# Kernel optimization log

Measured on AMD Instinct MI355X. Metric: run time of the kernel, lower is better.

## Reference

```python
import jax, jax.numpy as jnp
import numpy as np

TEMPERATURE = 0.1
B, T, D = 8, 1024, 1024
NEG_INF = -1e30

def setup_inputs() -> dict:
    key = jax.random.key(0)
    k1, k2, k3 = jax.random.split(key, 3)
    features = jax.random.normal(k1, (B, T, D), dtype=jnp.float32)
    masks = jax.random.bernoulli(k2, 0.05, (B, 1, T, T)).astype(jnp.float32)
    input_coords_length = jax.random.randint(k3, (B,), T // 2, T - 1)  # int32
    return {"features": features, "masks": masks, "input_coords_length": input_coords_length}


def _sup_con_loss(feat, mask, L):
    # feat: [T, D], mask: [T, T] float, L: scalar int valid length (slice [:L, :L])
    Tn = feat.shape[0]
    dt = feat.dtype
    vr = jnp.arange(Tn) < L                              # valid rows/cols [T]
    valid2d = (vr[:, None] & vr[None, :]).astype(dt)     # [T, T]
    dot = jnp.matmul(feat, feat.T) / TEMPERATURE         # [T, T]
    dot = jnp.where(vr[None, :], dot, NEG_INF)           # exclude padded cols from max
    logits = dot - jax.lax.stop_gradient(jnp.max(dot, axis=-1, keepdims=True))
    logits_mask = (1.0 - jnp.eye(Tn, dtype=dt)) * valid2d  # off-diagonal, in-slice
    exp_logits = jnp.exp(logits) * logits_mask
    m = mask * valid2d
    # negative_mask = 1-mask; entries < 1 zeroed (binary mask -> indicator of mask==0)
    neg = 1.0 - m
    neg = jnp.where(neg < 1.0, 0.0, neg) * valid2d
    # positive_mask = mask with entries > 0 set to 1
    pos = jnp.where(m > 0, 1.0, m)
    neg_denom = jnp.sum(exp_logits * neg, axis=-1, keepdims=True)
    pos_denom = jax.lax.stop_gradient(jnp.sum(exp_logits * pos, axis=-1, keepdims=True))
    log_prob = logits - jnp.log(neg_denom + pos_denom + 1e-6)
    m2 = m * logits_mask
    mean_log_prob_pos = (m2 * log_prob).sum(-1) / (m2.sum(-1) + 1e-6)  # [T]
    # mean over the L valid rows only (matches .mean() on the sliced tensor)
    return -jnp.sum(jnp.where(vr, mean_log_prob_pos, 0.0)) / L.astype(dt)


def _is_valid(mask, L):
    # valid sample iff sliced mask differs from eye(L) with [0,0]=0
    Tn = mask.shape[0]
    vr = jnp.arange(Tn) < L
    valid2d = (vr[:, None] & vr[None, :]).astype(mask.dtype)
    sanity = jnp.eye(Tn, dtype=mask.dtype).at[0, 0].set(0.0) * valid2d
    return jnp.any((mask * valid2d) != sanity)


def reference(features, masks, input_coords_length):
    L = input_coords_length + 1                      # [B]
    mask0 = masks[:, 0]                              # [B, T, T] (num_layers asserted == 1)
    losses = jax.vmap(_sup_con_loss)(features, mask0, L)   # [B]
    valid = jax.vmap(_is_valid)(mask0, L)                  # [B] bool
    vbs = jnp.maximum(jnp.sum(valid.astype(features.dtype)), 1.0)
    return jnp.sum(losses) / vbs
```

## Files before the change

### kernel.cpp

```cpp
#include <hip/hip_runtime.h>
#include <hip/hip_bf16.h>
#include <stdint.h>

#define T_DIM 1024
#define B_DIM 8

typedef __attribute__((ext_vector_type(8))) short short8;
typedef __attribute__((ext_vector_type(4))) float f32x4;

__device__ inline void gll16(const void* g, void* l) {
  __builtin_amdgcn_global_load_lds((__attribute__((address_space(1))) void*)g,
                                   (__attribute__((address_space(3))) void*)l,
                                   16, 0, 0);
}

__global__ __launch_bounds__(256) void convert_kernel(const float* __restrict__ F,
                                                      __hip_bfloat16* __restrict__ Fb) {
  const int t = blockIdx.x * 256 + threadIdx.x;
  const float4 v = ((const float4*)F)[t];
  union { __hip_bfloat16 h[4]; uint64_t u; } p;
  p.h[0] = __float2bfloat16(v.x);
  p.h[1] = __float2bfloat16(v.y);
  p.h[2] = __float2bfloat16(v.z);
  p.h[3] = __float2bfloat16(v.w);
  ((uint64_t*)Fb)[t] = p.u;
}

__global__ __launch_bounds__(512, 4) void fused_kernel(const __hip_bfloat16* __restrict__ Fb,
                                                       const float* __restrict__ M,
                                                       const int* __restrict__ icl,
                                                       float* __restrict__ part) {
  const int id = blockIdx.x;
  const int b  = id & 7;
  const int rt = (id >> 3) & 7;
  const int ct = id >> 6;
  const int L  = icl[b] + 1;
  if (rt * 128 >= L || ct * 128 >= L) return;

  __shared__ char smem[65536];
  __hip_bfloat16* As = (__hip_bfloat16*)smem;
  __hip_bfloat16* Bs = (__hip_bfloat16*)(smem + 32768);
  float* rp = (float*)smem;
  float* rp_m = rp;
  float* rp_d = rp + 512;
  float* rp_s = rp + 1024;
  float* rp_c = rp + 1536;
  float* rp_b = rp + 2048;

  const __hip_bfloat16* F = Fb + ((size_t)b << 20);
  const int tid  = threadIdx.x;
  const int lane = tid & 63;
  const int wave = tid >> 6;
  const int wrow = (wave >> 2) * 64;
  const int wcol = (wave & 3) * 32;
  const int row0 = rt * 128;
  const int col0 = ct * 128;

  const int fr = lane & 15;
  const int q  = lane >> 4;
  const int sl8 = (q ^ ((fr >> 1) & 3)) * 8;

  const int srow = tid >> 2;
  const int sgk  = (((tid & 3) ^ ((tid >> 3) & 3)) * 8);

  const size_t arow = (size_t)(row0 + srow) * T_DIM + sgk;
  const size_t brow = (size_t)(col0 + srow) * T_DIM + sgk;

  auto stage = [&](int buf, int step) {
    const int kb = step << 6;
#pragma unroll
    for (int p = 0; p < 2; p++)
      gll16(F + arow + kb + p * 32, As + buf * 8192 + p * 4096 + tid * 8);
#pragma unroll
    for (int p = 0; p < 2; p++)
      gll16(F + brow + kb + p * 32, Bs + buf * 8192 + p * 4096 + tid * 8);
  };

  stage(0, 0);
  stage(1, 1);

  f32x4 acc[4][2];
#pragma unroll
  for (int i = 0; i < 4; i++)
#pragma unroll
    for (int j = 0; j < 2; j++) acc[i][j] = (f32x4){0.f, 0.f, 0.f, 0.f};

#pragma unroll
  for (int t = 0; t < 16; ++t) {
    const int cur = t & 1;
    if (t < 15) { asm volatile("s_waitcnt vmcnt(4)" ::: "memory"); }
    else        { asm volatile("s_waitcnt vmcnt(0)" ::: "memory"); }
    __builtin_amdgcn_s_barrier();
    __builtin_amdgcn_sched_barrier(0);

    short8 af[2][4], bfr[2][2];
    const __hip_bfloat16* Ab = As + cur * 8192;
    const __hip_bfloat16* Bb = Bs + cur * 8192;
#pragma unroll
    for (int kk = 0; kk < 2; kk++) {
#pragma unroll
      for (int tt = 0; tt < 4; tt++)
        af[kk][tt] = *(const short8*)(Ab + kk * 4096 + (wrow + tt * 16 + fr) * 32 + sl8);
#pragma unroll
      for (int j = 0; j < 2; j++)
        bfr[kk][j] = *(const short8*)(Bb + kk * 4096 + (wcol + j * 16 + fr) * 32 + sl8);
    }
    asm volatile("s_waitcnt lgkmcnt(0)" ::: "memory");
    __builtin_amdgcn_sched_barrier(0);
    __builtin_amdgcn_s_barrier();
    __builtin_amdgcn_sched_barrier(0);

    if (t < 14) stage(cur, t + 2);

    __builtin_amdgcn_s_setprio(1);
#pragma unroll
    for (int kk = 0; kk < 2; kk++)
#pragma unroll
      for (int ti = 0; ti < 4; ti++)
#pragma unroll
        for (int tj = 0; tj < 2; tj++)
          acc[ti][tj] = __builtin_amdgcn_mfma_f32_16x16x32_bf16(bfr[kk][tj], af[kk][ti], acc[ti][tj], 0, 0, 0);
    __builtin_amdgcn_s_setprio(0);
  }
  __syncthreads();

  uint32_t mbits = 0;
  {
    const float* Mb = M + ((size_t)b << 20);
    union { float4 v; float f[4]; } mv[4][2];
#pragma unroll
    for (int ti = 0; ti < 4; ti++) {
      const int grow = row0 + wrow + ti * 16 + fr;
#pragma unroll
      for (int tj = 0; tj < 2; tj++)
        mv[ti][tj].v = *(const float4*)(Mb + ((size_t)grow << 10) + col0 + wcol + tj * 16 + q * 4);
    }
#pragma unroll
    for (int ti = 0; ti < 4; ti++)
#pragma unroll
      for (int tj = 0; tj < 2; tj++)
#pragma unroll
        for (int r = 0; r < 4; r++)
          mbits |= ((mv[ti][tj].f[r] != 0.f) ? 1u : 0u) << (ti * 8 + tj * 4 + r);
  }

#pragma unroll
  for (int ti = 0; ti < 4; ti++) {
    const int lrow = wrow + ti * 16 + fr;
    const int grow = row0 + lrow;
    float s[2][4];
#pragma unroll
    for (int tj = 0; tj < 2; tj++)
#pragma unroll
      for (int r = 0; r < 4; r++) {
        const int gcol = col0 + wcol + tj * 16 + q * 4 + r;
        s[tj][r] = (gcol < L) ? acc[ti][tj][r] * 10.0f : -1e30f;
      }
    float m = s[0][0];
#pragma unroll
    for (int tj = 0; tj < 2; tj++)
#pragma unroll
      for (int r = 0; r < 4; r++) m = fmaxf(m, s[tj][r]);
    m = fmaxf(m, __shfl_xor(m, 16, 64));
    m = fmaxf(m, __shfl_xor(m, 32, 64));

    float den = 0.f, msum = 0.f, cnt = 0.f, badf = 0.f;
#pragma unroll
    for (int tj = 0; tj < 2; tj++)
#pragma unroll
      for (int r = 0; r < 4; r++) {
        const int gcol = col0 + wcol + tj * 16 + q * 4 + r;
        if (gcol < L) {
          const float mk = (float)((mbits >> (ti * 8 + tj * 4 + r)) & 1u);
          if (gcol != grow) {
            den  += __expf(s[tj][r] - m);
            msum += mk * s[tj][r];
            cnt  += mk;
          }
          const float sane = (gcol == grow && grow != 0) ? 1.f : 0.f;
          badf = fmaxf(badf, (mk != sane) ? 1.f : 0.f);
        }
      }
    den  += __shfl_xor(den, 16, 64);  den  += __shfl_xor(den, 32, 64);
    msum += __shfl_xor(msum, 16, 64); msum += __shfl_xor(msum, 32, 64);
    cnt  += __shfl_xor(cnt, 16, 64);  cnt  += __shfl_xor(cnt, 32, 64);
    badf = fmaxf(badf, __shfl_xor(badf, 16, 64));
    badf = fmaxf(badf, __shfl_xor(badf, 32, 64));

    if (q == 0) {
      const int slot = wave & 3;
      rp_m[lrow * 4 + slot] = m;    rp_d[lrow * 4 + slot] = den;
      rp_s[lrow * 4 + slot] = msum; rp_c[lrow * 4 + slot] = cnt;
      rp_b[lrow * 4 + slot] = badf;
    }
  }
  __syncthreads();

  if (tid < 128) {
    float m = -1e30f;
#pragma unroll
    for (int s = 0; s < 4; s++) m = fmaxf(m, rp_m[tid * 4 + s]);
    float den = 0.f, msum = 0.f, cnt = 0.f, badf = 0.f;
#pragma unroll
    for (int s = 0; s < 4; s++) {
      den  += rp_d[tid * 4 + s] * __expf(rp_m[tid * 4 + s] - m);
      msum += rp_s[tid * 4 + s];
      cnt  += rp_c[tid * 4 + s];
      badf  = fmaxf(badf, rp_b[tid * 4 + s]);
    }
    float* p = part + ((((size_t)b * 1024 + row0 + tid) * 8) + ct) * 5;
    p[0] = m; p[1] = den; p[2] = msum; p[3] = cnt; p[4] = badf;
  }
}

__global__ __launch_bounds__(256) void reduce_kernel(const float* __restrict__ part,
                                                     const int* __restrict__ icl,
                                                     float* __restrict__ blk_sum,
                                                     int* __restrict__ blk_bad) {
  const int blk = blockIdx.x;
  const int row = blk * 256 + threadIdx.x;
  const int b = row >> 10;
  const int i = row & 1023;
  const int L = icl[b] + 1;
  float rv = 0.f;
  int bad = 0;
  if (i < L) {
    const float* p = part + (size_t)row * 40;
    const int ns = (L + 127) >> 7;
    float m = -1e30f;
    for (int s = 0; s < ns; s++) m = fmaxf(m, p[s * 5 + 0]);
    float den = 0.f, msum = 0.f, cnt = 0.f, badf = 0.f;
    for (int s = 0; s < ns; s++) {
      den  += p[s * 5 + 1] * __expf(p[s * 5 + 0] - m);
      msum += p[s * 5 + 2];
      cnt  += p[s * 5 + 3];
      badf  = fmaxf(badf, p[s * 5 + 4]);
    }
    const float A = msum - cnt * m;
    const float mlpp = (A - cnt * __logf(den + 1e-6f)) / (cnt + 1e-6f);
    rv = -mlpp / (float)L;
    bad = badf > 0.f ? 1 : 0;
  }
  const int tid  = threadIdx.x;
  const int lane = tid & 63;
  const int wave = tid >> 6;
  for (int o = 32; o > 0; o >>= 1) rv += __shfl_down(rv, o, 64);
  const int wbad = (__ballot(bad) != 0ull) ? 1 : 0;
  __shared__ float sred[4];
  __shared__ int bred[4];
  if (lane == 0) { sred[wave] = rv; bred[wave] = wbad; }
  __syncthreads();
  if (tid == 0) {
    blk_sum[blk] = sred[0] + sred[1] + sred[2] + sred[3];
    blk_bad[blk] = bred[0] | bred[1] | bred[2] | bred[3];
  }
}

__global__ __launch_bounds__(64) void final_kernel(const float* __restrict__ blk_sum,
                                                   const int* __restrict__ blk_bad,
                                                   float* __restrict__ out) {
  const int tid = threadIdx.x;
  float v = (tid < 32) ? blk_sum[tid] : 0.f;
  for (int o = 32; o > 0; o >>= 1) v += __shfl_down(v, o, 64);
  if (tid == 0) {
    int vcount = 0;
    for (int bb = 0; bb < B_DIM; bb++) {
      const int any = blk_bad[bb * 4] | blk_bad[bb * 4 + 1] |
                      blk_bad[bb * 4 + 2] | blk_bad[bb * 4 + 3];
      vcount += any ? 1 : 0;
    }
    out[0] = v / fmaxf((float)vcount, 1.0f);
  }
}

extern "C" void kernel_launch(void* const* d_in, const int* in_sizes, int n_in,
                              void* d_out, int out_size, void* d_ws, size_t ws_size,
                              hipStream_t stream) {
  const float* feat = (const float*)d_in[0];
  const float* mask = (const float*)d_in[1];
  const int*   icl  = (const int*)d_in[2];
  float* out = (float*)d_out;

  char* ws = (char*)d_ws;
  __hip_bfloat16* Fb = (__hip_bfloat16*)ws;
  float* part    = (float*)(ws + (16u << 20));
  float* blk_sum = (float*)(ws + (18u << 20));
  int*   blk_bad = (int*)(ws + (18u << 20) + 512);

  convert_kernel<<<dim3(8192), dim3(256), 0, stream>>>(feat, Fb);
  fused_kernel<<<dim3(512), dim3(512), 0, stream>>>(Fb, mask, icl, part);
  reduce_kernel<<<dim3(32), dim3(256), 0, stream>>>(part, icl, blk_sum, blk_bad);
  final_kernel<<<dim3(1), dim3(64), 0, stream>>>(blk_sum, blk_bad, out);
}
```

Measured before the change: 120.4 us.

## Fuse fp32-to-bf16 conversion into GEMM tile loads and share tile on diagonal blocks

Removes the separate convert kernel and its bf16 workspace. The fused kernel now loads fp32 features into registers, converts them to bf16 and writes them to LDS, using a register-staged double buffer in place of direct global-to-LDS loads. Diagonal tiles (row tile equals column tile) load and write only the A tile and reuse it as B. This saves a kernel launch and a full write and re-read of the bf16 copy. In exchange, each block reads twice the bytes in fp32, the conversion is redone by every block that uses a tile, and more registers are live, which may hurt occupancy or latency hiding.

```diff
diff --git a/kernel.cpp b/kernel.cpp
--- a/kernel.cpp
+++ b/kernel.cpp
@@ -8,25 +8,16 @@
 typedef __attribute__((ext_vector_type(8))) short short8;
 typedef __attribute__((ext_vector_type(4))) float f32x4;
 
-__device__ inline void gll16(const void* g, void* l) {
-  __builtin_amdgcn_global_load_lds((__attribute__((address_space(1))) void*)g,
-                                   (__attribute__((address_space(3))) void*)l,
-                                   16, 0, 0);
-}
-
-__global__ __launch_bounds__(256) void convert_kernel(const float* __restrict__ F,
-                                                      __hip_bfloat16* __restrict__ Fb) {
-  const int t = blockIdx.x * 256 + threadIdx.x;
-  const float4 v = ((const float4*)F)[t];
-  union { __hip_bfloat16 h[4]; uint64_t u; } p;
-  p.h[0] = __float2bfloat16(v.x);
-  p.h[1] = __float2bfloat16(v.y);
-  p.h[2] = __float2bfloat16(v.z);
-  p.h[3] = __float2bfloat16(v.w);
-  ((uint64_t*)Fb)[t] = p.u;
-}
-
-__global__ __launch_bounds__(512, 4) void fused_kernel(const __hip_bfloat16* __restrict__ Fb,
+__device__ inline short8 cvt8(const float4 a, const float4 b) {
+  union { __hip_bfloat16 h[8]; short8 s; } u;
+  u.h[0] = __float2bfloat16(a.x); u.h[1] = __float2bfloat16(a.y);
+  u.h[2] = __float2bfloat16(a.z); u.h[3] = __float2bfloat16(a.w);
+  u.h[4] = __float2bfloat16(b.x); u.h[5] = __float2bfloat16(b.y);
+  u.h[6] = __float2bfloat16(b.z); u.h[7] = __float2bfloat16(b.w);
+  return u.s;
+}
+
+__global__ __launch_bounds__(512, 4) void fused_kernel(const float* __restrict__ F32all,
                                                        const float* __restrict__ M,
                                                        const int* __restrict__ icl,
                                                        float* __restrict__ part) {
@@ -47,7 +38,7 @@
   float* rp_c = rp + 1536;
   float* rp_b = rp + 2048;
 
-  const __hip_bfloat16* F = Fb + ((size_t)b << 20);
+  const float* F32 = F32all + ((size_t)b << 20);
   const int tid  = threadIdx.x;
   const int lane = tid & 63;
   const int wave = tid >> 6;
@@ -55,6 +46,7 @@
   const int wcol = (wave & 3) * 32;
   const int row0 = rt * 128;
   const int col0 = ct * 128;
+  const bool diag = (rt == ct);
 
   const int fr = lane & 15;
   const int q  = lane >> 4;
@@ -63,54 +55,71 @@
   const int srow = tid >> 2;
   const int sgk  = (((tid & 3) ^ ((tid >> 3) & 3)) * 8);
 
-  const size_t arow = (size_t)(row0 + srow) * T_DIM + sgk;
-  const size_t brow = (size_t)(col0 + srow) * T_DIM + sgk;
-
-  auto stage = [&](int buf, int step) {
+  const float* Fa = F32 + (size_t)(row0 + srow) * T_DIM + sgk;
+  const float* Fc = F32 + (size_t)(col0 + srow) * T_DIM + sgk;
+
+  float4 ar[2][2], br[2][2];
+  auto loadT = [&](int step) {
     const int kb = step << 6;
 #pragma unroll
+    for (int p = 0; p < 2; p++) {
+      ar[p][0] = *(const float4*)(Fa + kb + p * 32);
+      ar[p][1] = *(const float4*)(Fa + kb + p * 32 + 4);
+    }
+    if (!diag) {
+#pragma unroll
+      for (int p = 0; p < 2; p++) {
+        br[p][0] = *(const float4*)(Fc + kb + p * 32);
+        br[p][1] = *(const float4*)(Fc + kb + p * 32 + 4);
+      }
+    }
+  };
+  auto writeT = [&](int buf) {
+#pragma unroll
     for (int p = 0; p < 2; p++)
-      gll16(F + arow + kb + p * 32, As + buf * 8192 + p * 4096 + tid * 8);
-#pragma unroll
-    for (int p = 0; p < 2; p++)
-      gll16(F + brow + kb + p * 32, Bs + buf * 8192 + p * 4096 + tid * 8);
+      *(short8*)(As + buf * 8192 + p * 4096 + tid * 8) = cvt8(ar[p][0], ar[p][1]);
+    if (!diag) {
+#pragma unroll
+      for (int p = 0; p < 2; p++)
+        *(short8*)(Bs + buf * 8192 + p * 4096 + tid * 8) = cvt8(br[p][0], br[p][1]);
+    }
   };
 
-  stage(0, 0);
-  stage(1, 1);
+  const __hip_bfloat16* Bbase = diag ? As : Bs;
 
   f32x4 acc[4][2];
 #pragma unroll
   for (int i = 0; i < 4; i++)
 #pragma unroll
     for (int j = 0; j < 2; j++) acc[i][j] = (f32x4){0.f, 0.f, 0.f, 0.f};
+
+  loadT(0);
+  writeT(0);
+  loadT(1);
 
 #pragma unroll
   for (int t = 0; t < 16; ++t) {
     const int cur = t & 1;
-    if (t < 15) { asm volatile("s_waitcnt vmcnt(4)" ::: "memory"); }
-    else        { asm volatile("s_waitcnt vmcnt(0)" ::: "memory"); }
-    __builtin_amdgcn_s_barrier();
-    __builtin_amdgcn_sched_barrier(0);
-
-    short8 af[2][4], bfr[2][2];
-    const __hip_bfloat16* Ab = As + cur * 8192;
-    const __hip_bfloat16* Bb = Bs + cur * 8192;
-#pragma unroll
-    for (int kk = 0; kk < 2; kk++) {
-#pragma unroll
-      for (int tt = 0; tt < 4; tt++)
-        af[kk][tt] = *(const short8*)(Ab + kk * 4096 + (wrow + tt * 16 + fr) * 32 + sl8);
-#pragma unroll
-      for (int j = 0; j < 2; j++)
-        bfr[kk][j] = *(const short8*)(Bb + kk * 4096 + (wcol + j * 16 + fr) * 32 + sl8);
-    }
     asm volatile("s_waitcnt lgkmcnt(0)" ::: "memory");
     __builtin_amdgcn_sched_barrier(0);
     __builtin_amdgcn_s_barrier();
     __builtin_amdgcn_sched_barrier(0);
 
-    if (t < 14) stage(cur, t + 2);
+    if (t < 15) writeT(cur ^ 1);
+    if (t < 14) loadT(t + 2);
+
+    short8 af[2][4], bfr[2][2];
+    const __hip_bfloat16* Ab = As + cur * 8192;
+    const __hip_bfloat16* Bb = Bbase + cur * 8192;
+#pragma unroll
+    for (int kk = 0; kk < 2; kk++) {
+#pragma unroll
+      for (int tt = 0; tt < 4; tt++)
+        af[kk][tt] = *(const short8*)(Ab + kk * 4096 + (wrow + tt * 16 + fr) * 32 + sl8);
+#pragma unroll
+      for (int j = 0; j < 2; j++)
+        bfr[kk][j] = *(const short8*)(Bb + kk * 4096 + (wcol + j * 16 + fr) * 32 + sl8);
+    }
 
     __builtin_amdgcn_s_setprio(1);
 #pragma unroll
@@ -282,13 +291,11 @@
   float* out = (float*)d_out;
 
   char* ws = (char*)d_ws;
-  __hip_bfloat16* Fb = (__hip_bfloat16*)ws;
-  float* part    = (float*)(ws + (16u << 20));
-  float* blk_sum = (float*)(ws + (18u << 20));
-  int*   blk_bad = (int*)(ws + (18u << 20) + 512);
-
-  convert_kernel<<<dim3(8192), dim3(256), 0, stream>>>(feat, Fb);
-  fused_kernel<<<dim3(512), dim3(512), 0, stream>>>(Fb, mask, icl, part);
+  float* part    = (float*)ws;
+  float* blk_sum = (float*)(ws + (2u << 20));
+  int*   blk_bad = (int*)(ws + (2u << 20) + 512);
+
+  fused_kernel<<<dim3(512), dim3(512), 0, stream>>>(feat, mask, icl, part);
   reduce_kernel<<<dim3(32), dim3(256), 0, stream>>>(part, icl, blk_sum, blk_bad);
   final_kernel<<<dim3(1), dim3(64), 0, stream>>>(blk_sum, blk_bad, out);
 }
```

After: 130.6 us. +8.5%, slower.

## Exploit Gram matrix symmetry to compute only upper-triangular tiles

Applied to the files above, without the earlier changes.

Uses the symmetry of feat·featᵀ so each block computes only tiles with rt<=ct, reducing the grid from 512 to 288 blocks. Off-diagonal tiles also produce the transposed tile's per-row softmax partials, reading the mask transposed and writing a second partial record. This roughly halves the matmul work. In exchange it adds uncoalesced transposed mask loads, extra shuffles and LDS reductions per block.

```diff
diff --git a/kernel.cpp b/kernel.cpp
--- a/kernel.cpp
+++ b/kernel.cpp
@@ -32,10 +32,12 @@
                                                        float* __restrict__ part) {
   const int id = blockIdx.x;
   const int b  = id & 7;
-  const int rt = (id >> 3) & 7;
-  const int ct = id >> 6;
+  int k = id >> 3;
+  int rt = 0;
+  while (k >= 8 - rt) { k -= 8 - rt; rt++; }
+  const int ct = rt + k;
   const int L  = icl[b] + 1;
-  if (rt * 128 >= L || ct * 128 >= L) return;
+  if (ct * 128 >= L) return;
 
   __shared__ char smem[65536];
   __hip_bfloat16* As = (__hip_bfloat16*)smem;
@@ -46,6 +48,12 @@
   float* rp_s = rp + 1024;
   float* rp_c = rp + 1536;
   float* rp_b = rp + 2048;
+  float* rp2  = rp + 2560;
+  float* rp2_m = rp2;
+  float* rp2_d = rp2 + 256;
+  float* rp2_s = rp2 + 512;
+  float* rp2_c = rp2 + 768;
+  float* rp2_b = rp2 + 1024;
 
   const __hip_bfloat16* F = Fb + ((size_t)b << 20);
   const int tid  = threadIdx.x;
@@ -55,6 +63,7 @@
   const int wcol = (wave & 3) * 32;
   const int row0 = rt * 128;
   const int col0 = ct * 128;
+  const bool diag = (rt == ct);
 
   const int fr = lane & 15;
   const int q  = lane >> 4;
@@ -194,6 +203,59 @@
       rp_b[lrow * 4 + slot] = badf;
     }
   }
+
+  if (!diag) {
+    const float* Mb = M + ((size_t)b << 20);
+    uint32_t mtbits = 0;
+#pragma unroll
+    for (int tj = 0; tj < 2; tj++)
+#pragma unroll
+      for (int r = 0; r < 4; r++) {
+        const int rowp = col0 + wcol + tj * 16 + q * 4 + r;
+#pragma unroll
+        for (int ti = 0; ti < 4; ti++) {
+          const int colp = row0 + wrow + ti * 16 + fr;
+          mtbits |= ((Mb[((size_t)rowp << 10) + colp] != 0.f) ? 1u : 0u)
+                    << ((tj * 4 + r) * 4 + ti);
+        }
+      }
+#pragma unroll
+    for (int tj = 0; tj < 2; tj++)
+#pragma unroll
+      for (int r = 0; r < 4; r++) {
+        const int gcol = col0 + wcol + tj * 16 + q * 4 + r;
+        float sv[4];
+#pragma unroll
+        for (int ti = 0; ti < 4; ti++)
+          sv[ti] = (gcol < L) ? acc[ti][tj][r] * 10.0f : -1e30f;
+        float mT = fmaxf(fmaxf(sv[0], sv[1]), fmaxf(sv[2], sv[3]));
+#pragma unroll
+        for (int d = 1; d < 16; d <<= 1) mT = fmaxf(mT, __shfl_xor(mT, d, 64));
+        float denT = 0.f, msumT = 0.f, cntT = 0.f, badT = 0.f;
+#pragma unroll
+        for (int ti = 0; ti < 4; ti++) {
+          const float mk = (float)((mtbits >> ((tj * 4 + r) * 4 + ti)) & 1u);
+          denT  += __expf(sv[ti] - mT);
+          msumT += mk * sv[ti];
+          cntT  += mk;
+          badT   = fmaxf(badT, mk);
+        }
+#pragma unroll
+        for (int d = 1; d < 16; d <<= 1) {
+          denT  += __shfl_xor(denT, d, 64);
+          msumT += __shfl_xor(msumT, d, 64);
+          cntT  += __shfl_xor(cntT, d, 64);
+          badT   = fmaxf(badT, __shfl_xor(badT, d, 64));
+        }
+        if (fr == 0) {
+          const int lrowp = wcol + tj * 16 + q * 4 + r;
+          const int slot = wave >> 2;
+          rp2_m[lrowp * 2 + slot] = mT;    rp2_d[lrowp * 2 + slot] = denT;
+          rp2_s[lrowp * 2 + slot] = msumT; rp2_c[lrowp * 2 + slot] = cntT;
+          rp2_b[lrowp * 2 + slot] = badT;
+        }
+      }
+  }
   __syncthreads();
 
   if (tid < 128) {
@@ -210,6 +272,19 @@
     }
     float* p = part + ((((size_t)b * 1024 + row0 + tid) * 8) + ct) * 5;
     p[0] = m; p[1] = den; p[2] = msum; p[3] = cnt; p[4] = badf;
+
+    if (!diag) {
+      const float m0 = rp2_m[tid * 2], m1 = rp2_m[tid * 2 + 1];
+      const float mT = fmaxf(m0, m1);
+      const float denT = rp2_d[tid * 2] * __expf(m0 - mT) +
+                         rp2_d[tid * 2 + 1] * __expf(m1 - mT);
+      float* p2 = part + ((((size_t)b * 1024 + col0 + tid) * 8) + rt) * 5;
+      p2[0] = mT;
+      p2[1] = denT;
+      p2[2] = rp2_s[tid * 2] + rp2_s[tid * 2 + 1];
+      p2[3] = rp2_c[tid * 2] + rp2_c[tid * 2 + 1];
+      p2[4] = fmaxf(rp2_b[tid * 2], rp2_b[tid * 2 + 1]);
+    }
   }
 }
 
@@ -288,7 +363,7 @@
   int*   blk_bad = (int*)(ws + (18u << 20) + 512);
 
   convert_kernel<<<dim3(8192), dim3(256), 0, stream>>>(feat, Fb);
-  fused_kernel<<<dim3(512), dim3(512), 0, stream>>>(Fb, mask, icl, part);
+  fused_kernel<<<dim3(288), dim3(512), 0, stream>>>(Fb, mask, icl, part);
   reduce_kernel<<<dim3(32), dim3(256), 0, stream>>>(part, icl, blk_sum, blk_bad);
   final_kernel<<<dim3(1), dim3(64), 0, stream>>>(blk_sum, blk_bad, out);
 }
```

Result: slower. 125.7 us (+4.5%).

## Exploit Gram matrix symmetry: compute upper-triangular tiles and mirror row stats

Applied to the files above, without the earlier changes.

The kernel now computes only the upper-triangular 128x64 tiles of the symmetric feature Gram matrix, using a triangular block index mapping, and emits per-row softmax partials for both the tile and its transpose. Mirrored tiles read the transposed mask with strided scalar loads and reduce column statistics across lanes and waves through shared memory. This roughly halves the MFMA and feature-load work, at the cost of uncoalesced mask reads, extra shuffles, and twice as many partial slots for the reduce kernel to process.

```diff
diff --git a/kernel.cpp b/kernel.cpp
--- a/kernel.cpp
+++ b/kernel.cpp
@@ -26,35 +26,37 @@
   ((uint64_t*)Fb)[t] = p.u;
 }
 
-__global__ __launch_bounds__(512, 4) void fused_kernel(const __hip_bfloat16* __restrict__ Fb,
+__global__ __launch_bounds__(256, 4) void fused_kernel(const __hip_bfloat16* __restrict__ Fb,
                                                        const float* __restrict__ M,
                                                        const int* __restrict__ icl,
                                                        float* __restrict__ part) {
   const int id = blockIdx.x;
   const int b  = id & 7;
-  const int rt = (id >> 3) & 7;
-  const int ct = id >> 6;
+  int k = id >> 3;
+  int rt = 0;
+  while (k >= 16 - 2 * rt) { k -= 16 - 2 * rt; rt++; }
+  const int ct2 = 2 * rt + k;
   const int L  = icl[b] + 1;
-  if (rt * 128 >= L || ct * 128 >= L) return;
-
-  __shared__ char smem[65536];
+  if (ct2 * 64 >= L) return;
+
+  __shared__ char smem[49152];
   __hip_bfloat16* As = (__hip_bfloat16*)smem;
   __hip_bfloat16* Bs = (__hip_bfloat16*)(smem + 32768);
-  float* rp = (float*)smem;
-  float* rp_m = rp;
-  float* rp_d = rp + 512;
-  float* rp_s = rp + 1024;
-  float* rp_c = rp + 1536;
-  float* rp_b = rp + 2048;
+  float* rp2 = (float*)smem;
+  float* rp2_m = rp2;
+  float* rp2_d = rp2 + 256;
+  float* rp2_s = rp2 + 512;
+  float* rp2_c = rp2 + 768;
+  float* rp2_b = rp2 + 1024;
 
   const __hip_bfloat16* F = Fb + ((size_t)b << 20);
   const int tid  = threadIdx.x;
   const int lane = tid & 63;
   const int wave = tid >> 6;
-  const int wrow = (wave >> 2) * 64;
-  const int wcol = (wave & 3) * 32;
+  const int wrow = wave * 32;
   const int row0 = rt * 128;
-  const int col0 = ct * 128;
+  const int col0 = ct2 * 64;
+  const bool mirror = (ct2 >= 2 * rt + 2);
 
   const int fr = lane & 15;
   const int q  = lane >> 4;
@@ -63,47 +65,47 @@
   const int srow = tid >> 2;
   const int sgk  = (((tid & 3) ^ ((tid >> 3) & 3)) * 8);
 
-  const size_t arow = (size_t)(row0 + srow) * T_DIM + sgk;
-  const size_t brow = (size_t)(col0 + srow) * T_DIM + sgk;
-
   auto stage = [&](int buf, int step) {
     const int kb = step << 6;
 #pragma unroll
-    for (int p = 0; p < 2; p++)
-      gll16(F + arow + kb + p * 32, As + buf * 8192 + p * 4096 + tid * 8);
-#pragma unroll
-    for (int p = 0; p < 2; p++)
-      gll16(F + brow + kb + p * 32, Bs + buf * 8192 + p * 4096 + tid * 8);
+    for (int kk = 0; kk < 2; kk++) {
+#pragma unroll
+      for (int h = 0; h < 2; h++)
+        gll16(F + (size_t)(row0 + h * 64 + srow) * T_DIM + kb + kk * 32 + sgk,
+              As + buf * 8192 + kk * 4096 + h * 2048 + tid * 8);
+      gll16(F + (size_t)(col0 + srow) * T_DIM + kb + kk * 32 + sgk,
+            Bs + buf * 4096 + kk * 2048 + tid * 8);
+    }
   };
 
   stage(0, 0);
   stage(1, 1);
 
-  f32x4 acc[4][2];
-#pragma unroll
-  for (int i = 0; i < 4; i++)
-#pragma unroll
-    for (int j = 0; j < 2; j++) acc[i][j] = (f32x4){0.f, 0.f, 0.f, 0.f};
+  f32x4 acc[2][4];
+#pragma unroll
+  for (int i = 0; i < 2; i++)
+#pragma unroll
+    for (int j = 0; j < 4; j++) acc[i][j] = (f32x4){0.f, 0.f, 0.f, 0.f};
 
 #pragma unroll
   for (int t = 0; t < 16; ++t) {
     const int cur = t & 1;
-    if (t < 15) { asm volatile("s_waitcnt vmcnt(4)" ::: "memory"); }
+    if (t < 15) { asm volatile("s_waitcnt vmcnt(6)" ::: "memory"); }
     else        { asm volatile("s_waitcnt vmcnt(0)" ::: "memory"); }
     __builtin_amdgcn_s_barrier();
     __builtin_amdgcn_sched_barrier(0);
 
-    short8 af[2][4], bfr[2][2];
+    short8 af[2][2], bfr[2][4];
     const __hip_bfloat16* Ab = As + cur * 8192;
-    const __hip_bfloat16* Bb = Bs + cur * 8192;
+    const __hip_bfloat16* Bb = Bs + cur * 4096;
 #pragma unroll
     for (int kk = 0; kk < 2; kk++) {
 #pragma unroll
-      for (int tt = 0; tt < 4; tt++)
-        af[kk][tt] = *(const short8*)(Ab + kk * 4096 + (wrow + tt * 16 + fr) * 32 + sl8);
-#pragma unroll
-      for (int j = 0; j < 2; j++)
-        bfr[kk][j] = *(const short8*)(Bb + kk * 4096 + (wcol + j * 16 + fr) * 32 + sl8);
+      for (int ti = 0; ti < 2; ti++)
+        af[kk][ti] = *(const short8*)(Ab + kk * 4096 + (wrow + ti * 16 + fr) * 32 + sl8);
+#pragma unroll
+      for (int tj = 0; tj < 4; tj++)
+        bfr[kk][tj] = *(const short8*)(Bb + kk * 2048 + (tj * 16 + fr) * 32 + sl8);
     }
     asm volatile("s_waitcnt lgkmcnt(0)" ::: "memory");
     __builtin_amdgcn_sched_barrier(0);
@@ -116,49 +118,49 @@
 #pragma unroll
     for (int kk = 0; kk < 2; kk++)
 #pragma unroll
-      for (int ti = 0; ti < 4; ti++)
-#pragma unroll
-        for (int tj = 0; tj < 2; tj++)
+      for (int ti = 0; ti < 2; ti++)
+#pragma unroll
+        for (int tj = 0; tj < 4; tj++)
           acc[ti][tj] = __builtin_amdgcn_mfma_f32_16x16x32_bf16(bfr[kk][tj], af[kk][ti], acc[ti][tj], 0, 0, 0);
     __builtin_amdgcn_s_setprio(0);
   }
   __syncthreads();
 
+  const float* Mb = M + ((size_t)b << 20);
+
   uint32_t mbits = 0;
   {
-    const float* Mb = M + ((size_t)b << 20);
-    union { float4 v; float f[4]; } mv[4][2];
-#pragma unroll
-    for (int ti = 0; ti < 4; ti++) {
+    union { float4 v; float f[4]; } mv[2][4];
+#pragma unroll
+    for (int ti = 0; ti < 2; ti++) {
       const int grow = row0 + wrow + ti * 16 + fr;
 #pragma unroll
-      for (int tj = 0; tj < 2; tj++)
-        mv[ti][tj].v = *(const float4*)(Mb + ((size_t)grow << 10) + col0 + wcol + tj * 16 + q * 4);
-    }
-#pragma unroll
-    for (int ti = 0; ti < 4; ti++)
-#pragma unroll
-      for (int tj = 0; tj < 2; tj++)
+      for (int tj = 0; tj < 4; tj++)
+        mv[ti][tj].v = *(const float4*)(Mb + ((size_t)grow << 10) + col0 + tj * 16 + q * 4);
+    }
+#pragma unroll
+    for (int ti = 0; ti < 2; ti++)
+#pragma unroll
+      for (int tj = 0; tj < 4; tj++)
 #pragma unroll
         for (int r = 0; r < 4; r++)
-          mbits |= ((mv[ti][tj].f[r] != 0.f) ? 1u : 0u) << (ti * 8 + tj * 4 + r);
-  }
-
-#pragma unroll
-  for (int ti = 0; ti < 4; ti++) {
-    const int lrow = wrow + ti * 16 + fr;
-    const int grow = row0 + lrow;
-    float s[2][4];
-#pragma unroll
-    for (int tj = 0; tj < 2; tj++)
+          mbits |= ((mv[ti][tj].f[r] != 0.f) ? 1u : 0u) << (ti * 16 + tj * 4 + r);
+  }
+
+#pragma unroll
+  for (int ti = 0; ti < 2; ti++) {
+    const int grow = row0 + wrow + ti * 16 + fr;
+    float s[4][4];
+#pragma unroll
+    for (int tj = 0; tj < 4; tj++)
 #pragma unroll
       for (int r = 0; r < 4; r++) {
-        const int gcol = col0 + wcol + tj * 16 + q * 4 + r;
+        const int gcol = col0 + tj * 16 + q * 4 + r;
         s[tj][r] = (gcol < L) ? acc[ti][tj][r] * 10.0f : -1e30f;
       }
     float m = s[0][0];
 #pragma unroll
-    for (int tj = 0; tj < 2; tj++)
+    for (int tj = 0; tj < 4; tj++)
 #pragma unroll
       for (int r = 0; r < 4; r++) m = fmaxf(m, s[tj][r]);
     m = fmaxf(m, __shfl_xor(m, 16, 64));
@@ -166,12 +168,12 @@
 
     float den = 0.f, msum = 0.f, cnt = 0.f, badf = 0.f;
 #pragma unroll
-    for (int tj = 0; tj < 2; tj++)
+    for (int tj = 0; tj < 4; tj++)
 #pragma unroll
       for (int r = 0; r < 4; r++) {
-        const int gcol = col0 + wcol + tj * 16 + q * 4 + r;
+        const int gcol = col0 + tj * 16 + q * 4 + r;
         if (gcol < L) {
-          const float mk = (float)((mbits >> (ti * 8 + tj * 4 + r)) & 1u);
+          const float mk = (float)((mbits >> (ti * 16 + tj * 4 + r)) & 1u);
           if (gcol != grow) {
             den  += __expf(s[tj][r] - m);
             msum += mk * s[tj][r];
@@ -187,29 +189,72 @@
     badf = fmaxf(badf, __shfl_xor(badf, 16, 64));
     badf = fmaxf(badf, __shfl_xor(badf, 32, 64));
 
-    if (q == 0) {
-      const int slot = wave & 3;
-      rp_m[lrow * 4 + slot] = m;    rp_d[lrow * 4 + slot] = den;
-      rp_s[lrow * 4 + slot] = msum; rp_c[lrow * 4 + slot] = cnt;
-      rp_b[lrow * 4 + slot] = badf;
-    }
+    if (lane < 16) {
+      float* p = part + ((((size_t)b * 1024 + grow) * 16) + ct2) * 5;
+      p[0] = m; p[1] = den; p[2] = msum; p[3] = cnt; p[4] = badf;
+    }
+  }
+
+  if (mirror) {
+    uint32_t mtbits = 0;
+#pragma unroll
+    for (int tj = 0; tj < 4; tj++)
+#pragma unroll
+      for (int r = 0; r < 4; r++) {
+        const int rowp = col0 + tj * 16 + q * 4 + r;
+#pragma unroll
+        for (int ti = 0; ti < 2; ti++) {
+          const int colp = row0 + wrow + ti * 16 + fr;
+          mtbits |= ((Mb[((size_t)rowp << 10) + colp] != 0.f) ? 1u : 0u)
+                    << ((tj * 4 + r) * 2 + ti);
+        }
+      }
+#pragma unroll
+    for (int tj = 0; tj < 4; tj++)
+#pragma unroll
+      for (int r = 0; r < 4; r++) {
+        const float sv0 = acc[0][tj][r] * 10.0f;
+        const float sv1 = acc[1][tj][r] * 10.0f;
+        float mT = fmaxf(sv0, sv1);
+#pragma unroll
+        for (int d = 1; d < 16; d <<= 1) mT = fmaxf(mT, __shfl_xor(mT, d, 64));
+        const float mk0 = (float)((mtbits >> ((tj * 4 + r) * 2)) & 1u);
+        const float mk1 = (float)((mtbits >> ((tj * 4 + r) * 2 + 1)) & 1u);
+        float denT  = __expf(sv0 - mT) + __expf(sv1 - mT);
+        float msumT = mk0 * sv0 + mk1 * sv1;
+        float cntT  = mk0 + mk1;
+        float badT  = fmaxf(mk0, mk1);
+#pragma unroll
+        for (int d = 1; d < 16; d <<= 1) {
+          denT  += __shfl_xor(denT, d, 64);
+          msumT += __shfl_xor(msumT, d, 64);
+          cntT  += __shfl_xor(cntT, d, 64);
+          badT   = fmaxf(badT, __shfl_xor(badT, d, 64));
+        }
+        if (fr == 0) {
+          const int lrowp = tj * 16 + q * 4 + r;
+          rp2_m[lrowp * 4 + wave] = mT;    rp2_d[lrowp * 4 + wave] = denT;
+          rp2_s[lrowp * 4 + wave] = msumT; rp2_c[lrowp * 4 + wave] = cntT;
+          rp2_b[lrowp * 4 + wave] = badT;
+        }
+      }
   }
   __syncthreads();
 
-  if (tid < 128) {
-    float m = -1e30f;
-#pragma unroll
-    for (int s = 0; s < 4; s++) m = fmaxf(m, rp_m[tid * 4 + s]);
-    float den = 0.f, msum = 0.f, cnt = 0.f, badf = 0.f;
-#pragma unroll
-    for (int s = 0; s < 4; s++) {
-      den  += rp_d[tid * 4 + s] * __expf(rp_m[tid * 4 + s] - m);
-      msum += rp_s[tid * 4 + s];
-      cnt  += rp_c[tid * 4 + s];
-      badf  = fmaxf(badf, rp_b[tid * 4 + s]);
-    }
-    float* p = part + ((((size_t)b * 1024 + row0 + tid) * 8) + ct) * 5;
-    p[0] = m; p[1] = den; p[2] = msum; p[3] = cnt; p[4] = badf;
+  if (mirror && tid < 64) {
+#pragma unroll
+    for (int pr = 0; pr < 2; pr++) {
+      const float m0 = rp2_m[tid * 4 + pr * 2], m1 = rp2_m[tid * 4 + pr * 2 + 1];
+      const float mT = fmaxf(m0, m1);
+      const float denT = rp2_d[tid * 4 + pr * 2] * __expf(m0 - mT) +
+                         rp2_d[tid * 4 + pr * 2 + 1] * __expf(m1 - mT);
+      float* p2 = part + ((((size_t)b * 1024 + col0 + tid) * 16) + (2 * rt + pr)) * 5;
+      p2[0] = mT;
+      p2[1] = denT;
+      p2[2] = rp2_s[tid * 4 + pr * 2] + rp2_s[tid * 4 + pr * 2 + 1];
+      p2[3] = rp2_c[tid * 4 + pr * 2] + rp2_c[tid * 4 + pr * 2 + 1];
+      p2[4] = fmaxf(rp2_b[tid * 4 + pr * 2], rp2_b[tid * 4 + pr * 2 + 1]);
+    }
   }
 }
 
@@ -225,8 +270,8 @@
   float rv = 0.f;
   int bad = 0;
   if (i < L) {
-    const float* p = part + (size_t)row * 40;
-    const int ns = (L + 127) >> 7;
+    const float* p = part + (size_t)row * 80;
+    const int ns = (L + 63) >> 6;
     float m = -1e30f;
     for (int s = 0; s < ns; s++) m = fmaxf(m, p[s * 5 + 0]);
     float den = 0.f, msum = 0.f, cnt = 0.f, badf = 0.f;
@@ -284,11 +329,11 @@
   char* ws = (char*)d_ws;
   __hip_bfloat16* Fb = (__hip_bfloat16*)ws;
   float* part    = (float*)(ws + (16u << 20));
-  float* blk_sum = (float*)(ws + (18u << 20));
-  int*   blk_bad = (int*)(ws + (18u << 20) + 512);
+  float* blk_sum = (float*)(ws + (19u << 20));
+  int*   blk_bad = (int*)(ws + (19u << 20) + 512);
 
   convert_kernel<<<dim3(8192), dim3(256), 0, stream>>>(feat, Fb);
-  fused_kernel<<<dim3(512), dim3(512), 0, stream>>>(Fb, mask, icl, part);
+  fused_kernel<<<dim3(576), dim3(256), 0, stream>>>(Fb, mask, icl, part);
   reduce_kernel<<<dim3(32), dim3(256), 0, stream>>>(part, icl, blk_sum, blk_bad);
   final_kernel<<<dim3(1), dim3(64), 0, stream>>>(blk_sum, blk_bad, out);
 }
```

Result: slower. 131.0 us (+8.8%).
